# Kernel optimization log

Hardware: AMD Instinct MI355X
Metric: run time of the kernel (lower is better)

## Reference

```python
import jax, jax.numpy as jnp
import numpy as np

K = 12

@jax.custom_vjp
def spike(v_scaled):
    # Heaviside with straight surrogate gradient (triangular) on backward
    return jnp.where(v_scaled > 0, jnp.ones_like(v_scaled), jnp.zeros_like(v_scaled))

def _spike_fwd(v_scaled):
    return spike(v_scaled), v_scaled

def _spike_bwd(v_scaled, g):
    return (g * jnp.maximum(1.0 - jnp.abs(v_scaled), 0.0),)

spike.defvjp(_spike_fwd, _spike_bwd)


def setup_inputs() -> dict:
    key = jax.random.key(0)
    k0, k1, k2, k3 = jax.random.split(key, 4)
    x = jax.random.normal(k0, (32, 128, 56, 56), dtype=jnp.float32)
    h = jax.random.uniform(k1, (K,), dtype=jnp.float32, minval=-1.0, maxval=0.0)
    d = jax.random.uniform(k2, (K,), dtype=jnp.float32, minval=-0.5, maxval=1.0)
    T = jax.random.uniform(k3, (K,), dtype=jnp.float32, minval=-1.0, maxval=1.0)
    return {"x": x, "h": h, "d": d, "T": T}


def reference(x, h, d, T):
    zero = jnp.asarray(0.0, x.dtype)

    def step(carry, params):
        v, z, out, v_reg, z_reg = carry
        ht, dt, Tt = params
        v = v - z * ht
        v_scaled = (v - Tt) / (jnp.abs(v) + 1.0)
        z = spike(v_scaled)
        v_reg = v_reg + jnp.square(jnp.mean(jnp.maximum(jnp.abs(v_scaled) - 1.0, 0.0)))
        z_reg = z_reg + jnp.mean(z)
        out = out + z * dt
        return (v, z, out, v_reg, z_reg), None

    init = (x, jnp.zeros_like(x), jnp.zeros_like(x), zero, zero)
    (v, z, out, v_reg, z_reg), _ = jax.lax.scan(step, init, (h, d, T))
    return out, v_reg, z_reg
```

## Files before the change

kernel.cpp:

```cpp
#include <hip/hip_runtime.h>
#include <math.h>

#define KSTEPS 12
#define ITERS  4

typedef float f32x4 __attribute__((ext_vector_type(4)));

__device__ __forceinline__ unsigned omap(float f) {
    unsigned u = __float_as_uint(f);
    return (u & 0x80000000u) ? ~u : (u | 0x80000000u);
}
__device__ __forceinline__ float ounmap(unsigned o) {
    unsigned bits = (o & 0x80000000u) ? (o ^ 0x80000000u) : ~o;
    return __uint_as_float(bits);
}

__device__ __forceinline__ int sim_mask(float x, const float* hh, const float* TT) {
    float v = x, zf = 0.f;
    int mask = 0;
#pragma unroll
    for (int t = 0; t < KSTEPS; ++t) {
        v  = fmaf(-hh[t], zf, v);
        zf = (v > TT[t]) ? 1.f : 0.f;
        mask |= (v > TT[t] ? 1 : 0) << t;
    }
    return mask;
}

__global__ void fsc_setup(const float* __restrict__ h, const float* __restrict__ d,
                          const float* __restrict__ T, float* __restrict__ tbl) {
    __shared__ float thRaw[KSTEPS];
    __shared__ int   rank[KSTEPS];
    float hh[KSTEPS], dd[KSTEPS], TT[KSTEPS];
#pragma unroll
    for (int t = 0; t < KSTEPS; ++t) { hh[t] = h[t]; dd[t] = d[t]; TT[t] = T[t]; }

    const int lane = threadIdx.x;
    if (lane < KSTEPS) {
        unsigned lo = omap(-128.0f), hi = omap(128.0f);
        float th;
        if (sim_mask(ounmap(lo), hh, TT) >> lane & 1)         th = -INFINITY;
        else if (!(sim_mask(ounmap(hi), hh, TT) >> lane & 1)) th = INFINITY;
        else {
            while (hi - lo > 1u) {
                unsigned mid = lo + (hi - lo) / 2u;
                if (sim_mask(ounmap(mid), hh, TT) >> lane & 1) hi = mid;
                else                                           lo = mid;
            }
            th = ounmap(lo);
        }
        thRaw[lane] = th;
    }
    __syncthreads();
    if (lane < KSTEPS) {
        const float th = thRaw[lane];
        int r = 0;
#pragma unroll
        for (int j = 0; j < KSTEPS; ++j) {
            const float oj = thRaw[j];
            if (oj < th || (oj == th && j < lane)) r++;
        }
        rank[lane] = r;
        tbl[r] = th;
    }
    __syncthreads();
    if (lane < KSTEPS + 1) {
        float o = 0.f;
#pragma unroll
        for (int t = 0; t < KSTEPS; ++t) {
            const float zf = (rank[t] < lane) ? 1.f : 0.f;
            o = fmaf(dd[t], zf, o);
        }
        const unsigned b = (__float_as_uint(o) & ~15u) | (unsigned)lane;
        tbl[KSTEPS + lane] = __uint_as_float(b);
    }
}

__global__ __launch_bounds__(256) void fsc_main(
    const f32x4* __restrict__ x, const float* __restrict__ tbl,
    f32x4* __restrict__ out, float* __restrict__ partial, int n4)
{
    const int tid    = blockIdx.x * blockDim.x + threadIdx.x;
    const int stride = gridDim.x * blockDim.x;
    int cnt = 0;

    float th[KSTEPS], val[KSTEPS + 1];
#pragma unroll
    for (int m = 0; m < KSTEPS; ++m) th[m] = tbl[m];
#pragma unroll
    for (int k = 0; k <= KSTEPS; ++k) val[k] = tbl[KSTEPS + k];

    if (tid + (ITERS - 1) * stride < n4) {
        f32x4 xv[ITERS];
#pragma unroll
        for (int u = 0; u < ITERS; ++u) xv[u] = x[tid + u * stride];
#pragma unroll
        for (int u = 0; u < ITERS; ++u) {
            f32x4 ov;
#pragma unroll
            for (int j = 0; j < 4; ++j) {
                const float xj = xv[u][j];
                float e = val[0];
#pragma unroll
                for (int m = 0; m < KSTEPS; ++m)
                    e = (xj > th[m]) ? val[m + 1] : e;
                ov[j] = e;
                cnt += (int)(__float_as_uint(e) & 15u);
            }
            __builtin_nontemporal_store(ov, &out[tid + u * stride]);
        }
    } else {
        for (int i = tid; i < n4; i += stride) {
            const f32x4 xv = x[i];
            f32x4 ov;
#pragma unroll
            for (int j = 0; j < 4; ++j) {
                const float xj = xv[j];
                float e = val[0];
#pragma unroll
                for (int m = 0; m < KSTEPS; ++m)
                    e = (xj > th[m]) ? val[m + 1] : e;
                ov[j] = e;
                cnt += (int)(__float_as_uint(e) & 15u);
            }
            __builtin_nontemporal_store(ov, &out[i]);
        }
    }

    const int lane = threadIdx.x & 63;
    const int wv   = threadIdx.x >> 6;
    __shared__ int smi[4];
#pragma unroll
    for (int off = 32; off > 0; off >>= 1) cnt += __shfl_down(cnt, off);
    if (lane == 0) smi[wv] = cnt;
    __syncthreads();
    if (threadIdx.x == 0)
        partial[blockIdx.x] = (float)(smi[0] + smi[1] + smi[2] + smi[3]);
}

__global__ __launch_bounds__(256) void fsc_finalize(
    const float* __restrict__ partial, int nblocks,
    float* __restrict__ out_tail, double inv_n)
{
    double acc = 0.0;
    for (int b = threadIdx.x; b < nblocks; b += blockDim.x)
        acc += (double)partial[b];
    const int lane = threadIdx.x & 63;
    const int wv   = threadIdx.x >> 6;
    __shared__ double sm[4];
#pragma unroll
    for (int off = 32; off > 0; off >>= 1) acc += __shfl_down(acc, off);
    if (lane == 0) sm[wv] = acc;
    __syncthreads();
    if (threadIdx.x == 0) {
        const double tot = sm[0] + sm[1] + sm[2] + sm[3];
        out_tail[0] = 0.0f;
        out_tail[1] = (float)(tot * inv_n);
    }
}

extern "C" void kernel_launch(void* const* d_in, const int* in_sizes, int n_in,
                              void* d_out, int out_size, void* d_ws, size_t ws_size,
                              hipStream_t stream) {
    const f32x4*  x    = (const f32x4*)d_in[0];
    const float*  h    = (const float*)d_in[1];
    const float*  dpar = (const float*)d_in[2];
    const float*  T    = (const float*)d_in[3];
    float* out = (float*)d_out;

    const int n  = in_sizes[0];
    const int n4 = n / 4;
    const int blocks = (n4 + 256 * ITERS - 1) / (256 * ITERS);

    float* tbl     = (float*)d_ws;
    float* partial = (float*)d_ws + 64;

    fsc_setup   <<<1,      64,  0, stream>>>(h, dpar, T, tbl);
    fsc_main    <<<blocks, 256, 0, stream>>>(x, tbl, (f32x4*)out, partial, n4);
    fsc_finalize<<<1,      256, 0, stream>>>(partial, blocks, out + n, 1.0 / (double)n);
}
```

Measured before the change: 35.78 us.

## Fuse threshold-table setup into main kernel, computed per block in shared memory

Removes the separate single-block setup kernel and its launch by having the first wavefront of every block redo the threshold binary search and value table into shared memory. The x loads are issued before the setup so global memory latency overlaps with the table computation. In exchange, every block repeats the serial binary search (about 32 iterations of a 12-step simulation), adding per-block latency. It also relies on wave-level waitcnt instead of barriers for the intra-wave shared-memory ordering.

```diff
diff --git a/kernel.cpp b/kernel.cpp
--- a/kernel.cpp
+++ b/kernel.cpp
@@ -27,73 +27,81 @@
     return mask;
 }
 
-__global__ void fsc_setup(const float* __restrict__ h, const float* __restrict__ d,
-                          const float* __restrict__ T, float* __restrict__ tbl) {
-    __shared__ float thRaw[KSTEPS];
-    __shared__ int   rank[KSTEPS];
-    float hh[KSTEPS], dd[KSTEPS], TT[KSTEPS];
-#pragma unroll
-    for (int t = 0; t < KSTEPS; ++t) { hh[t] = h[t]; dd[t] = d[t]; TT[t] = T[t]; }
-
-    const int lane = threadIdx.x;
-    if (lane < KSTEPS) {
-        unsigned lo = omap(-128.0f), hi = omap(128.0f);
-        float th;
-        if (sim_mask(ounmap(lo), hh, TT) >> lane & 1)         th = -INFINITY;
-        else if (!(sim_mask(ounmap(hi), hh, TT) >> lane & 1)) th = INFINITY;
-        else {
-            while (hi - lo > 1u) {
-                unsigned mid = lo + (hi - lo) / 2u;
-                if (sim_mask(ounmap(mid), hh, TT) >> lane & 1) hi = mid;
-                else                                           lo = mid;
-            }
-            th = ounmap(lo);
-        }
-        thRaw[lane] = th;
-    }
-    __syncthreads();
-    if (lane < KSTEPS) {
-        const float th = thRaw[lane];
-        int r = 0;
-#pragma unroll
-        for (int j = 0; j < KSTEPS; ++j) {
-            const float oj = thRaw[j];
-            if (oj < th || (oj == th && j < lane)) r++;
-        }
-        rank[lane] = r;
-        tbl[r] = th;
-    }
-    __syncthreads();
-    if (lane < KSTEPS + 1) {
-        float o = 0.f;
-#pragma unroll
-        for (int t = 0; t < KSTEPS; ++t) {
-            const float zf = (rank[t] < lane) ? 1.f : 0.f;
-            o = fmaf(dd[t], zf, o);
-        }
-        const unsigned b = (__float_as_uint(o) & ~15u) | (unsigned)lane;
-        tbl[KSTEPS + lane] = __uint_as_float(b);
-    }
-}
-
 __global__ __launch_bounds__(256) void fsc_main(
-    const f32x4* __restrict__ x, const float* __restrict__ tbl,
+    const f32x4* __restrict__ x,
+    const float* __restrict__ h,
+    const float* __restrict__ d,
+    const float* __restrict__ T,
     f32x4* __restrict__ out, float* __restrict__ partial, int n4)
 {
     const int tid    = blockIdx.x * blockDim.x + threadIdx.x;
     const int stride = gridDim.x * blockDim.x;
-    int cnt = 0;
+
+    const bool fast = (tid + (ITERS - 1) * stride < n4);
+    f32x4 xv[ITERS];
+    if (fast) {
+#pragma unroll
+        for (int u = 0; u < ITERS; ++u) xv[u] = x[tid + u * stride];
+    }
+
+    __shared__ float thRaw[KSTEPS];
+    __shared__ int   rank[KSTEPS];
+    __shared__ float sTh[KSTEPS], sVal[KSTEPS + 1];
+
+    if (threadIdx.x < 64) {
+        const int lane = threadIdx.x;
+        float hh[KSTEPS], dd[KSTEPS], TT[KSTEPS];
+#pragma unroll
+        for (int t = 0; t < KSTEPS; ++t) { hh[t] = h[t]; dd[t] = d[t]; TT[t] = T[t]; }
+        if (lane < KSTEPS) {
+            unsigned lo = omap(-128.0f), hi = omap(128.0f);
+            float th;
+            if (sim_mask(ounmap(lo), hh, TT) >> lane & 1)         th = -INFINITY;
+            else if (!(sim_mask(ounmap(hi), hh, TT) >> lane & 1)) th = INFINITY;
+            else {
+                while (hi - lo > 1u) {
+                    unsigned mid = lo + (hi - lo) / 2u;
+                    if (sim_mask(ounmap(mid), hh, TT) >> lane & 1) hi = mid;
+                    else                                           lo = mid;
+                }
+                th = ounmap(lo);
+            }
+            thRaw[lane] = th;
+        }
+        __builtin_amdgcn_s_waitcnt(0);
+        if (lane < KSTEPS) {
+            const float th = thRaw[lane];
+            int r = 0;
+#pragma unroll
+            for (int j = 0; j < KSTEPS; ++j) {
+                const float oj = thRaw[j];
+                if (oj < th || (oj == th && j < lane)) r++;
+            }
+            rank[lane] = r;
+            sTh[r] = th;
+        }
+        __builtin_amdgcn_s_waitcnt(0);
+        if (lane < KSTEPS + 1) {
+            float o = 0.f;
+#pragma unroll
+            for (int t = 0; t < KSTEPS; ++t) {
+                const float zf = (rank[t] < lane) ? 1.f : 0.f;
+                o = fmaf(dd[t], zf, o);
+            }
+            const unsigned b = (__float_as_uint(o) & ~15u) | (unsigned)lane;
+            sVal[lane] = __uint_as_float(b);
+        }
+    }
+    __syncthreads();
 
     float th[KSTEPS], val[KSTEPS + 1];
 #pragma unroll
-    for (int m = 0; m < KSTEPS; ++m) th[m] = tbl[m];
+    for (int m = 0; m < KSTEPS; ++m) th[m] = sTh[m];
 #pragma unroll
-    for (int k = 0; k <= KSTEPS; ++k) val[k] = tbl[KSTEPS + k];
+    for (int k = 0; k <= KSTEPS; ++k) val[k] = sVal[k];
 
-    if (tid + (ITERS - 1) * stride < n4) {
-        f32x4 xv[ITERS];
-#pragma unroll
-        for (int u = 0; u < ITERS; ++u) xv[u] = x[tid + u * stride];
+    int cnt = 0;
+    if (fast) {
 #pragma unroll
         for (int u = 0; u < ITERS; ++u) {
             f32x4 ov;
@@ -111,11 +119,11 @@
         }
     } else {
         for (int i = tid; i < n4; i += stride) {
-            const f32x4 xv = x[i];
+            const f32x4 xw = x[i];
             f32x4 ov;
 #pragma unroll
             for (int j = 0; j < 4; ++j) {
-                const float xj = xv[j];
+                const float xj = xw[j];
                 float e = val[0];
 #pragma unroll
                 for (int m = 0; m < KSTEPS; ++m)
@@ -172,10 +180,8 @@
     const int n4 = n / 4;
     const int blocks = (n4 + 256 * ITERS - 1) / (256 * ITERS);
 
-    float* tbl     = (float*)d_ws;
-    float* partial = (float*)d_ws + 64;
+    float* partial = (float*)d_ws;
 
-    fsc_setup   <<<1,      64,  0, stream>>>(h, dpar, T, tbl);
-    fsc_main    <<<blocks, 256, 0, stream>>>(x, tbl, (f32x4*)out, partial, n4);
+    fsc_main    <<<blocks, 256, 0, stream>>>(x, h, dpar, T, (f32x4*)out, partial, n4);
     fsc_finalize<<<1,      256, 0, stream>>>(partial, blocks, out + n, 1.0 / (double)n);
 }
```

Result: slower. 40.07 us (+12.0%).
